# Performance work log

Hardware: AMD Instinct MI355X
Metric: run time of the kernel (lower is better)

The kernel has to match this reference:

```python
import jax, jax.numpy as jnp
import numpy as np

N_NODES = 100000
N_EDGES = 1600000
N_GRAPHS = 1024
TIME_DIM = 64
HID = 32
HEADS = 4
NEG_SLOPE = 0.2


def _gat_layer(x, src, dst, W, a_src, a_dst, bias, heads, out_dim):
    # PyG GATConv: h = x @ W, per-head attention, segment softmax over incoming edges at dst.
    N = x.shape[0]
    h = (x @ W).reshape(N, heads, out_dim)                     # [N, H, D]
    alpha_src = jnp.sum(h * a_src, axis=-1)                    # [N, H]
    alpha_dst = jnp.sum(h * a_dst, axis=-1)                    # [N, H]
    e = alpha_src[src] + alpha_dst[dst]                        # [E, H]
    e = jnp.where(e > 0, e, NEG_SLOPE * e)                     # LeakyReLU(0.2)
    m = jax.ops.segment_max(e, dst, num_segments=N)            # [N, H]
    m = jnp.where(jnp.isfinite(m), m, 0.0)
    ex = jnp.exp(e - m[dst])                                   # [E, H]
    s = jax.ops.segment_sum(ex, dst, num_segments=N)           # [N, H]
    alpha = ex / (s[dst] + 1e-16)                              # [E, H]
    msg = h[src] * alpha[..., None]                            # [E, H, D]
    out = jax.ops.segment_sum(msg, dst, num_segments=N)        # [N, H, D]
    return out.reshape(N, heads * out_dim) + bias


def setup_inputs() -> dict:
    key = jax.random.key(0)
    ks = jax.random.split(key, 12)
    x = jax.random.normal(ks[0], (N_NODES, TIME_DIM), jnp.float32)
    edge_index = jax.random.randint(ks[1], (2, N_EDGES), 0, N_NODES, jnp.int32)
    batch = jnp.sort(jax.random.randint(ks[2], (N_NODES,), 0, N_GRAPHS, jnp.int32))
    s = 0.1
    params = {
        "W1": jax.random.normal(ks[3], (TIME_DIM, HEADS * HID), jnp.float32) * s,
        "a_src1": jax.random.normal(ks[4], (HEADS, HID), jnp.float32) * s,
        "a_dst1": jax.random.normal(ks[5], (HEADS, HID), jnp.float32) * s,
        "b1": jnp.zeros((HEADS * HID,), jnp.float32),
        "W2": jax.random.normal(ks[6], (HEADS * HID, HID), jnp.float32) * s,
        "a_src2": jax.random.normal(ks[7], (1, HID), jnp.float32) * s,
        "a_dst2": jax.random.normal(ks[8], (1, HID), jnp.float32) * s,
        "b2": jnp.zeros((HID,), jnp.float32),
        "Wc": jax.random.normal(ks[9], (HID, 1), jnp.float32) * s,
        "bc": jnp.zeros((1,), jnp.float32),
    }
    return dict(x=x, edge_index=edge_index, batch=batch, **params)


def reference(x, edge_index, batch, W1, a_src1, a_dst1, b1, W2, a_src2, a_dst2, b2, Wc, bc):
    N = x.shape[0]
    # PyG GATConv adds self-loops by default.
    loops = jnp.arange(N, dtype=edge_index.dtype)
    src = jnp.concatenate([edge_index[0], loops])
    dst = jnp.concatenate([edge_index[1], loops])

    h1 = jax.nn.relu(_gat_layer(x, src, dst, W1, a_src1, a_dst1, b1, HEADS, HID))
    h2 = jax.nn.relu(_gat_layer(h1, src, dst, W2, a_src2, a_dst2, b2, 1, HID))

    # global_mean_pool over batch ids
    sums = jax.ops.segment_sum(h2, batch, num_segments=N_GRAPHS)          # [G, HID]
    cnts = jax.ops.segment_sum(jnp.ones((N,), h2.dtype), batch, num_segments=N_GRAPHS)
    pooled = sums / jnp.maximum(cnts, 1.0)[:, None]

    return jax.nn.sigmoid(pooled @ Wc + bc)                               # [G, 1]
```

## Files before the change

### kernel.cpp

```cpp
#include <hip/hip_runtime.h>
#include <hip/hip_bf16.h>

#define BSH 7
#define MAXNB 800
#define STILE 4096
#define BCAP 4096

__device__ inline float bf_lo(unsigned u) { return __uint_as_float(u << 16); }
__device__ inline float bf_hi(unsigned u) { return __uint_as_float(u & 0xffff0000u); }
__device__ inline unsigned bfpack(float x, float y) {
    unsigned lo = (unsigned)__bfloat16_as_ushort(__float2bfloat16(x));
    unsigned hi = ((unsigned)__bfloat16_as_ushort(__float2bfloat16(y))) << 16;
    return lo | hi;
}

__device__ inline void fp4fma(unsigned u, float w, float* a) {
    auto f0 = __builtin_amdgcn_cvt_scalef32_pk_f32_fp4(u, 1.0f, 0);
    auto f1 = __builtin_amdgcn_cvt_scalef32_pk_f32_fp4(u, 1.0f, 1);
    auto f2 = __builtin_amdgcn_cvt_scalef32_pk_f32_fp4(u, 1.0f, 2);
    auto f3 = __builtin_amdgcn_cvt_scalef32_pk_f32_fp4(u, 1.0f, 3);
    a[0] = fmaf(w, f0[0], a[0]); a[1] = fmaf(w, f0[1], a[1]);
    a[2] = fmaf(w, f1[0], a[2]); a[3] = fmaf(w, f1[1], a[3]);
    a[4] = fmaf(w, f2[0], a[4]); a[5] = fmaf(w, f2[1], a[5]);
    a[6] = fmaf(w, f3[0], a[6]); a[7] = fmaf(w, f3[1], a[7]);
}


__global__ __launch_bounds__(256) void k_front(const int* __restrict__ ei, int E, int NB,
                                               int* __restrict__ bcur, int* __restrict__ pairs,
                                               const float* __restrict__ x, const float* __restrict__ W1,
                                               const float* __restrict__ asw, const float* __restrict__ adw,
                                               unsigned* __restrict__ h4, unsigned* __restrict__ aPq,
                                               float2* __restrict__ aDp, int N, int nbsc) {
    __shared__ union USm {
        struct { int lh[MAXNB]; int lbase[MAXNB]; } sc;
        float xt[64][36];
    } sm;
    int t = threadIdx.x;
    if (blockIdx.x < nbsc) {
        int e0 = blockIdx.x * STILE;
        int e1 = min(E, e0 + STILE);
        for (int i = t; i < NB; i += 256) sm.sc.lh[i] = 0;
        __syncthreads();
        int myd[16];
        int q = 0;
        for (int e = e0 + t; e < e1; e += 256, q++) {
            int d = ei[E + e];
            myd[q] = d;
            atomicAdd(&sm.sc.lh[d >> BSH], 1);
        }
        __syncthreads();
        for (int i = t; i < NB; i += 256) {
            int c = sm.sc.lh[i];
            sm.sc.lbase[i] = c ? atomicAdd(&bcur[i], c) : 0;
        }
        __syncthreads();
        for (int i = t; i < NB; i += 256) sm.sc.lh[i] = 0;
        __syncthreads();
        q = 0;
        for (int e = e0 + t; e < e1; e += 256, q++) {
            int s = ei[e];
            int d = myd[q];
            int bk = d >> BSH;
            int off = atomicAdd(&sm.sc.lh[bk], 1);
            pairs[(size_t)bk * BCAP + sm.sc.lbase[bk] + off] = (s << BSH) | (d & ((1 << BSH) - 1));
        }
        return;
    }
    int n0 = (blockIdx.x - nbsc) * 32;
    for (int i = t; i < 32 * 64; i += 256) {
        int r = i >> 6, k = i & 63;
        sm.xt[k][r] = (n0 + r < N) ? x[(size_t)(n0 + r) * 64 + k] : 0.f;
    }
    __syncthreads();
    int cg = t & 31, rg = t >> 5;
    int c0 = cg * 4, r0 = rg * 4;
    int head = c0 >> 5;
    const float* Wp = W1 + c0;
    float acc[4][4];
#pragma unroll
    for (int r = 0; r < 4; r++)
#pragma unroll
        for (int c = 0; c < 4; c++) acc[r][c] = 0.f;
#pragma unroll 4
    for (int k = 0; k < 64; k++) {
        float4 wv = *(const float4*)(Wp + (size_t)k * 128);
        float4 xv = *(const float4*)&sm.xt[k][r0];
        float xr;
        xr = xv.x; acc[0][0]=fmaf(xr,wv.x,acc[0][0]); acc[0][1]=fmaf(xr,wv.y,acc[0][1]); acc[0][2]=fmaf(xr,wv.z,acc[0][2]); acc[0][3]=fmaf(xr,wv.w,acc[0][3]);
        xr = xv.y; acc[1][0]=fmaf(xr,wv.x,acc[1][0]); acc[1][1]=fmaf(xr,wv.y,acc[1][1]); acc[1][2]=fmaf(xr,wv.z,acc[1][2]); acc[1][3]=fmaf(xr,wv.w,acc[1][3]);
        xr = xv.z; acc[2][0]=fmaf(xr,wv.x,acc[2][0]); acc[2][1]=fmaf(xr,wv.y,acc[2][1]); acc[2][2]=fmaf(xr,wv.z,acc[2][2]); acc[2][3]=fmaf(xr,wv.w,acc[2][3]);
        xr = xv.w; acc[3][0]=fmaf(xr,wv.x,acc[3][0]); acc[3][1]=fmaf(xr,wv.y,acc[3][1]); acc[3][2]=fmaf(xr,wv.z,acc[3][2]); acc[3][3]=fmaf(xr,wv.w,acc[3][3]);
    }
#pragma unroll
    for (int r = 0; r < 4; r++) {
        int n = n0 + r0 + r;
        if (n < N) {
            unsigned u = __builtin_amdgcn_cvt_scalef32_pk_fp4_f32(0u, acc[r][0], acc[r][1], 1.0f, 0);
            u = __builtin_amdgcn_cvt_scalef32_pk_fp4_f32(u, acc[r][2], acc[r][3], 1.0f, 1);
            ((unsigned short*)h4)[(size_t)n * 32 + cg] = (unsigned short)(u & 0xffffu);
        }
    }
    float4 awv = *(const float4*)(asw + c0);
    float4 dwv = *(const float4*)(adw + c0);
#pragma unroll
    for (int r = 0; r < 4; r++) {
        float as = acc[r][0] * awv.x + acc[r][1] * awv.y + acc[r][2] * awv.z + acc[r][3] * awv.w;
        float ad = acc[r][0] * dwv.x + acc[r][1] * dwv.y + acc[r][2] * dwv.z + acc[r][3] * dwv.w;
#pragma unroll
        for (int m = 1; m < 8; m <<= 1) { as += __shfl_xor(as, m); ad += __shfl_xor(ad, m); }
        int n = n0 + r0 + r;
        if ((t & 7) == 0 && n < N) {
            aPq[n * 4 + head] = bfpack(__expf(as), __expf(0.2f * as));
            aDp[n * 4 + head] = make_float2(__expf(ad), __expf(0.2f * ad));
        }
    }
}


__global__ __launch_bounds__(256) void k_build(const int* __restrict__ pairs,
                                               const int* __restrict__ bcur, int N, int NB,
                                               int2* __restrict__ span, int* __restrict__ csr) {
    __shared__ int lcnt[128];
    __shared__ int loff[128];
    __shared__ int lcur[128];
    int b = blockIdx.x, t = threadIdx.x;
    int node0 = b << BSH;
    size_t base = (size_t)b * BCAP;
    int ne = bcur[b];
    if (t < 128) lcnt[t] = 0;
    __syncthreads();
    for (int i = t; i < ne; i += 256) atomicAdd(&lcnt[pairs[base + i] & 127], 1);
    __syncthreads();
    if (t < 128) loff[t] = lcnt[t];
    __syncthreads();
#pragma unroll
    for (int off = 1; off < 128; off <<= 1) {
        int v = (t < 128 && t >= off) ? loff[t - off] : 0;
        __syncthreads();
        if (t < 128) loff[t] += v;
        __syncthreads();
    }
    if (t < 128) {
        int excl = loff[t] - lcnt[t];
        int n = node0 + t;
        if (n < N) span[n] = make_int2((int)base + excl, (int)base + excl + lcnt[t]);
        lcur[t] = excl;
    }
    __syncthreads();
    for (int i = t; i < ne; i += 256) {
        int p = pairs[base + i];
        int pos = (int)base + atomicAdd(&lcur[p & 127], 1);
        csr[pos] = ((unsigned)p) >> BSH;
    }
}


__global__ __launch_bounds__(256) void k_gat1(const unsigned* __restrict__ h4,
                                              const unsigned* __restrict__ aPq, const float2* __restrict__ aDp,
                                              const int2* __restrict__ span, const int* __restrict__ csr,
                                              const float* __restrict__ b1, unsigned* __restrict__ out, int N) {
    int t = threadIdx.x;
    int n = blockIdx.x * 4 + (t >> 6);
    if (n >= N) return;
    int lane = t & 63;
    int e4 = lane >> 4, c = lane & 15;
    int head = c >> 2;
    float2 dnp = aDp[n * 4 + head];
    float ec = dnp.x, ed = dnp.y;
    unsigned apn = aPq[n * 4 + head];
    float w_self = fmaxf(bf_lo(apn) * ec, bf_hi(apn) * ed);
    int2 sp = span[n];
    int beg = sp.x, end = sp.y;

    float a[8] = {0, 0, 0, 0, 0, 0, 0, 0};
    float s = 0.f;
    if (e4 == 0) {
        fp4fma(h4[(size_t)n * 16 + c], w_self, a);
        s = w_self;
    }
    int j = beg + e4;
    for (; j + 4 < end; j += 8) {
        int s0 = csr[j], s1 = csr[j + 4];
        unsigned ap0 = aPq[s0 * 4 + head], ap1 = aPq[s1 * 4 + head];
        unsigned u0 = h4[(size_t)s0 * 16 + c];
        unsigned u1 = h4[(size_t)s1 * 16 + c];
        float w0 = fmaxf(bf_lo(ap0) * ec, bf_hi(ap0) * ed);
        float w1 = fmaxf(bf_lo(ap1) * ec, bf_hi(ap1) * ed);
        s += w0 + w1;
        fp4fma(u0, w0, a);
        fp4fma(u1, w1, a);
    }
    for (; j < end; j += 4) {
        int sj = csr[j];
        unsigned ap = aPq[sj * 4 + head];
        unsigned u = h4[(size_t)sj * 16 + c];
        float w = fmaxf(bf_lo(ap) * ec, bf_hi(ap) * ed);
        s += w;
        fp4fma(u, w, a);
    }
#pragma unroll
    for (int off = 16; off < 64; off <<= 1) {
#pragma unroll
        for (int i = 0; i < 8; i++) a[i] += __shfl_xor(a[i], off);
        s += __shfl_xor(s, off);
    }
    if (e4 == 0) {
        float inv = 1.f / (s + 1e-16f);
        float4 ba = ((const float4*)b1)[c * 2];
        float4 bb = ((const float4*)b1)[c * 2 + 1];
        float o0 = fmaxf(fmaf(a[0], inv, ba.x), 0.f);
        float o1 = fmaxf(fmaf(a[1], inv, ba.y), 0.f);
        float o2 = fmaxf(fmaf(a[2], inv, ba.z), 0.f);
        float o3 = fmaxf(fmaf(a[3], inv, ba.w), 0.f);
        float o4 = fmaxf(fmaf(a[4], inv, bb.x), 0.f);
        float o5 = fmaxf(fmaf(a[5], inv, bb.y), 0.f);
        float o6 = fmaxf(fmaf(a[6], inv, bb.z), 0.f);
        float o7 = fmaxf(fmaf(a[7], inv, bb.w), 0.f);
        uint4 o;
        o.x = bfpack(o0, o1); o.y = bfpack(o2, o3);
        o.z = bfpack(o4, o5); o.w = bfpack(o6, o7);
        ((uint4*)out)[(size_t)n * 16 + c] = o;
    }
}


__global__ __launch_bounds__(256) void k_gemm2(const unsigned* __restrict__ h1b, const float* __restrict__ W2,
                                               const float* __restrict__ asw, const float* __restrict__ adw,
                                               unsigned short* __restrict__ h4b, unsigned* __restrict__ aPq,
                                               float2* __restrict__ aDp, int N) {
    __shared__ float xt[128][36];
    int t = threadIdx.x;
    int n0 = blockIdx.x * 32;
    for (int i = t; i < 32 * 64; i += 256) {
        int r = i >> 6, c = i & 63;
        unsigned u = (n0 + r < N) ? h1b[(size_t)(n0 + r) * 64 + c] : 0u;
        xt[2 * c][r]     = bf_lo(u);
        xt[2 * c + 1][r] = bf_hi(u);
    }
    __syncthreads();
    int cg = t & 7, rg = t >> 3;
    int c0 = cg * 4;
    const float* Wp = W2 + c0;
    float a0 = 0.f, a1 = 0.f, a2 = 0.f, a3 = 0.f;
#pragma unroll 4
    for (int k = 0; k < 128; k++) {
        float4 wv = *(const float4*)(Wp + (size_t)k * 32);
        float xr = xt[k][rg];
        a0 = fmaf(xr, wv.x, a0); a1 = fmaf(xr, wv.y, a1);
        a2 = fmaf(xr, wv.z, a2); a3 = fmaf(xr, wv.w, a3);
    }
    int n = n0 + rg;
    if (n < N) {
        unsigned u = __builtin_amdgcn_cvt_scalef32_pk_fp4_f32(0u, a0, a1, 1.0f, 0);
        u = __builtin_amdgcn_cvt_scalef32_pk_fp4_f32(u, a2, a3, 1.0f, 1);
        h4b[(size_t)n * 8 + cg] = (unsigned short)(u & 0xffffu);
    }
    float4 awv = *(const float4*)(asw + c0);
    float4 dwv = *(const float4*)(adw + c0);
    float as = a0 * awv.x + a1 * awv.y + a2 * awv.z + a3 * awv.w;
    float ad = a0 * dwv.x + a1 * dwv.y + a2 * dwv.z + a3 * dwv.w;
#pragma unroll
    for (int m = 1; m < 8; m <<= 1) { as += __shfl_xor(as, m); ad += __shfl_xor(ad, m); }
    if (cg == 0 && n < N) {
        aPq[n] = bfpack(__expf(as), __expf(0.2f * as));
        aDp[n] = make_float2(__expf(ad), __expf(0.2f * ad));
    }
}


__global__ __launch_bounds__(256) void k_gat2(const unsigned* __restrict__ h4,
                                              const unsigned* __restrict__ aPq, const float2* __restrict__ aDp,
                                              const int2* __restrict__ span, const int* __restrict__ csr,
                                              const float* __restrict__ b2, float* __restrict__ out, int N) {
    int t = threadIdx.x;
    int n = blockIdx.x * 4 + (t >> 6);
    if (n >= N) return;
    int lane = t & 63;
    int e16 = lane >> 2, c = lane & 3;
    float2 dnp = aDp[n];
    float ec = dnp.x, ed = dnp.y;
    unsigned apn = aPq[n];
    float w_self = fmaxf(bf_lo(apn) * ec, bf_hi(apn) * ed);
    int2 sp = span[n];
    int beg = sp.x, end = sp.y;

    float a[8] = {0, 0, 0, 0, 0, 0, 0, 0};
    float s = 0.f;
    if (e16 == 0) {
        fp4fma(h4[(size_t)n * 4 + c], w_self, a);
        s = w_self;
    }
    int j = beg + e16;
    for (; j + 16 < end; j += 32) {
        int s0 = csr[j], s1 = csr[j + 16];
        unsigned ap0 = aPq[s0], ap1 = aPq[s1];
        unsigned u0 = h4[(size_t)s0 * 4 + c];
        unsigned u1 = h4[(size_t)s1 * 4 + c];
        float w0 = fmaxf(bf_lo(ap0) * ec, bf_hi(ap0) * ed);
        float w1 = fmaxf(bf_lo(ap1) * ec, bf_hi(ap1) * ed);
        s += w0 + w1;
        fp4fma(u0, w0, a);
        fp4fma(u1, w1, a);
    }
    for (; j < end; j += 16) {
        int sj = csr[j];
        unsigned ap = aPq[sj];
        unsigned u = h4[(size_t)sj * 4 + c];
        float w = fmaxf(bf_lo(ap) * ec, bf_hi(ap) * ed);
        s += w;
        fp4fma(u, w, a);
    }
#pragma unroll
    for (int off = 4; off < 64; off <<= 1) {
#pragma unroll
        for (int i = 0; i < 8; i++) a[i] += __shfl_xor(a[i], off);
        s += __shfl_xor(s, off);
    }
    if (e16 == 0) {
        float inv = 1.f / (s + 1e-16f);
        float4 ba = ((const float4*)b2)[c * 2];
        float4 bb = ((const float4*)b2)[c * 2 + 1];
        float4 oa, ob;
        oa.x = fmaxf(fmaf(a[0], inv, ba.x), 0.f);
        oa.y = fmaxf(fmaf(a[1], inv, ba.y), 0.f);
        oa.z = fmaxf(fmaf(a[2], inv, ba.z), 0.f);
        oa.w = fmaxf(fmaf(a[3], inv, ba.w), 0.f);
        ob.x = fmaxf(fmaf(a[4], inv, bb.x), 0.f);
        ob.y = fmaxf(fmaf(a[5], inv, bb.y), 0.f);
        ob.z = fmaxf(fmaf(a[6], inv, bb.z), 0.f);
        ob.w = fmaxf(fmaf(a[7], inv, bb.w), 0.f);
        ((float4*)out)[(size_t)n * 8 + c * 2]     = oa;
        ((float4*)out)[(size_t)n * 8 + c * 2 + 1] = ob;
    }
}


__global__ void k_pool(const float* __restrict__ h2r, const int* __restrict__ batch, int N,
                       const float* __restrict__ Wc, const float* __restrict__ bc,
                       float* __restrict__ out) {
    int g = blockIdx.x;
    int t = threadIdx.x, d = t & 31, r = t >> 5;
    int lo = 0, hi = N;
    while (lo < hi) { int mid = (lo + hi) >> 1; if (batch[mid] < g) lo = mid + 1; else hi = mid; }
    int start = lo;
    hi = N;
    while (lo < hi) { int mid = (lo + hi) >> 1; if (batch[mid] < g + 1) lo = mid + 1; else hi = mid; }
    int end = lo;
    float sum = 0.f;
    for (int i = start + r; i < end; i += 2) sum += h2r[(size_t)i * 32 + d];
    sum += __shfl_xor(sum, 32);
    float cnt = (float)(end - start);
    float mean = sum / fmaxf(cnt, 1.f);
    float v = mean * Wc[d];
#pragma unroll
    for (int m = 16; m >= 1; m >>= 1) v += __shfl_xor(v, m);
    if (t == 0) out[g] = 1.f / (1.f + expf(-(v + bc[0])));
}


extern "C" void kernel_launch(void* const* d_in, const int* in_sizes, int n_in,
                              void* d_out, int out_size, void* d_ws, size_t ws_size,
                              hipStream_t stream) {
    const float* x    = (const float*)d_in[0];
    const int*   ei   = (const int*)d_in[1];
    const int*   batch= (const int*)d_in[2];
    const float* W1   = (const float*)d_in[3];
    const float* as1  = (const float*)d_in[4];
    const float* ad1  = (const float*)d_in[5];
    const float* b1   = (const float*)d_in[6];
    const float* W2   = (const float*)d_in[7];
    const float* as2  = (const float*)d_in[8];
    const float* ad2  = (const float*)d_in[9];
    const float* b2   = (const float*)d_in[10];
    const float* Wc   = (const float*)d_in[11];
    const float* bc   = (const float*)d_in[12];

    const int N = in_sizes[0] / 64;
    const int E = in_sizes[1] / 2;
    const int G = out_size;
    const int NB = (N + 127) >> BSH;

    size_t off = 0;
    char* base = (char*)d_ws;
    auto alloc = [&](size_t bytes) -> char* {
        char* p = base + off;
        off += (bytes + 255) & ~(size_t)255;
        return p;
    };
    int*      bcur  = (int*)alloc((size_t)NB * 4);
    int*      pairs = (int*)alloc((size_t)NB * BCAP * 4);
    int2*     span  = (int2*)alloc((size_t)N * 8);
    int*      csr   = (int*)alloc((size_t)NB * BCAP * 4);
    unsigned* h4_1  = (unsigned*)alloc((size_t)N * 64);
    unsigned* h1b   = (unsigned*)alloc((size_t)N * 64 * 4);
    unsigned* aPq1  = (unsigned*)alloc((size_t)N * 4 * 4);
    float2*   aDp1  = (float2*)alloc((size_t)N * 4 * 8);
    unsigned short* h4_2 = (unsigned short*)alloc((size_t)N * 16);
    unsigned* aPq2  = (unsigned*)alloc((size_t)N * 4);
    float2*   aDp2  = (float2*)alloc((size_t)N * 8);
    float*    h2r   = (float*)alloc((size_t)N * 32 * 4);
    (void)ws_size; (void)n_in;

    const int nbsc = (E + STILE - 1) / STILE;

    hipMemsetAsync(bcur, 0, (size_t)NB * 4, stream);

    k_front<<<nbsc + (N + 31) / 32, 256, 0, stream>>>(ei, E, NB, bcur, pairs,
                                                      x, W1, as1, ad1, h4_1, aPq1, aDp1, N, nbsc);
    k_build<<<NB, 256, 0, stream>>>(pairs, bcur, N, NB, span, csr);

    k_gat1<<<(N + 3) / 4, 256, 0, stream>>>(h4_1, aPq1, aDp1, span, csr, b1, h1b, N);

    k_gemm2<<<(N + 31) / 32, 256, 0, stream>>>(h1b, W2, as2, ad2, h4_2, aPq2, aDp2, N);
    k_gat2<<<(N + 3) / 4, 256, 0, stream>>>((const unsigned*)h4_2, aPq2, aDp2, span, csr, b2, h2r, N);

    k_pool<<<G, 64, 0, stream>>>(h2r, batch, N, Wc, bc, (float*)d_out);
}
```

Baseline: 247.9 us.

## Split fused scatter/GEMM front kernel and double edge tile size

Splits the combined bucket-scatter and layer-1 GEMM kernel into two separate kernels, launching the GEMM after the CSR build instead of alongside the scatter. It also doubles the per-block edge tile from 4096 to 8192, which halves the number of scatter blocks and the global atomics on bucket counters. The trade-off is the lost overlap between scatter and GEMM blocks plus one extra launch. The larger myd register array (32 entries) may raise register pressure and lower occupancy in the scatter kernel.

```diff
diff --git a/kernel.cpp b/kernel.cpp
--- a/kernel.cpp
+++ b/kernel.cpp
@@ -3,7 +3,7 @@
 
 #define BSH 7
 #define MAXNB 800
-#define STILE 4096
+#define STILE 8192
 #define BCAP 4096
 
 __device__ inline float bf_lo(unsigned u) { return __uint_as_float(u << 16); }
@@ -26,51 +26,51 @@
 }
 
 
-__global__ __launch_bounds__(256) void k_front(const int* __restrict__ ei, int E, int NB,
-                                               int* __restrict__ bcur, int* __restrict__ pairs,
-                                               const float* __restrict__ x, const float* __restrict__ W1,
+__global__ __launch_bounds__(256) void k_bscatter(const int* __restrict__ ei, int E, int NB,
+                                                  int* __restrict__ bcur, int* __restrict__ pairs) {
+    __shared__ int lh[MAXNB];
+    __shared__ int lbase[MAXNB];
+    int t = threadIdx.x;
+    int e0 = blockIdx.x * STILE;
+    int e1 = min(E, e0 + STILE);
+    for (int i = t; i < NB; i += 256) lh[i] = 0;
+    __syncthreads();
+    int myd[32];
+    int q = 0;
+    for (int e = e0 + t; e < e1; e += 256, q++) {
+        int d = ei[E + e];
+        myd[q] = d;
+        atomicAdd(&lh[d >> BSH], 1);
+    }
+    __syncthreads();
+    for (int i = t; i < NB; i += 256) {
+        int c = lh[i];
+        lbase[i] = c ? atomicAdd(&bcur[i], c) : 0;
+    }
+    __syncthreads();
+    for (int i = t; i < NB; i += 256) lh[i] = 0;
+    __syncthreads();
+    q = 0;
+    for (int e = e0 + t; e < e1; e += 256, q++) {
+        int s = ei[e];
+        int d = myd[q];
+        int bk = d >> BSH;
+        int off = atomicAdd(&lh[bk], 1);
+        pairs[(size_t)bk * BCAP + lbase[bk] + off] = (s << BSH) | (d & ((1 << BSH) - 1));
+    }
+}
+
+
+__global__ __launch_bounds__(256) void k_gemm1(const float* __restrict__ x, const float* __restrict__ W1,
                                                const float* __restrict__ asw, const float* __restrict__ adw,
                                                unsigned* __restrict__ h4, unsigned* __restrict__ aPq,
-                                               float2* __restrict__ aDp, int N, int nbsc) {
-    __shared__ union USm {
-        struct { int lh[MAXNB]; int lbase[MAXNB]; } sc;
-        float xt[64][36];
-    } sm;
+                                               float2* __restrict__ aDp, int N) {
+    __shared__ float xt[64][36];
     int t = threadIdx.x;
-    if (blockIdx.x < nbsc) {
-        int e0 = blockIdx.x * STILE;
-        int e1 = min(E, e0 + STILE);
-        for (int i = t; i < NB; i += 256) sm.sc.lh[i] = 0;
-        __syncthreads();
-        int myd[16];
-        int q = 0;
-        for (int e = e0 + t; e < e1; e += 256, q++) {
-            int d = ei[E + e];
-            myd[q] = d;
-            atomicAdd(&sm.sc.lh[d >> BSH], 1);
-        }
-        __syncthreads();
-        for (int i = t; i < NB; i += 256) {
-            int c = sm.sc.lh[i];
-            sm.sc.lbase[i] = c ? atomicAdd(&bcur[i], c) : 0;
-        }
-        __syncthreads();
-        for (int i = t; i < NB; i += 256) sm.sc.lh[i] = 0;
-        __syncthreads();
-        q = 0;
-        for (int e = e0 + t; e < e1; e += 256, q++) {
-            int s = ei[e];
-            int d = myd[q];
-            int bk = d >> BSH;
-            int off = atomicAdd(&sm.sc.lh[bk], 1);
-            pairs[(size_t)bk * BCAP + sm.sc.lbase[bk] + off] = (s << BSH) | (d & ((1 << BSH) - 1));
-        }
-        return;
-    }
-    int n0 = (blockIdx.x - nbsc) * 32;
+    int n0 = blockIdx.x * 32;
     for (int i = t; i < 32 * 64; i += 256) {
         int r = i >> 6, k = i & 63;
-        sm.xt[k][r] = (n0 + r < N) ? x[(size_t)(n0 + r) * 64 + k] : 0.f;
+        xt[k][r] = (n0 + r < N) ? x[(size_t)(n0 + r) * 64 + k] : 0.f;
     }
     __syncthreads();
     int cg = t & 31, rg = t >> 5;
@@ -85,7 +85,7 @@
 #pragma unroll 4
     for (int k = 0; k < 64; k++) {
         float4 wv = *(const float4*)(Wp + (size_t)k * 128);
-        float4 xv = *(const float4*)&sm.xt[k][r0];
+        float4 xv = *(const float4*)&xt[k][r0];
         float xr;
         xr = xv.x; acc[0][0]=fmaf(xr,wv.x,acc[0][0]); acc[0][1]=fmaf(xr,wv.y,acc[0][1]); acc[0][2]=fmaf(xr,wv.z,acc[0][2]); acc[0][3]=fmaf(xr,wv.w,acc[0][3]);
         xr = xv.y; acc[1][0]=fmaf(xr,wv.x,acc[1][0]); acc[1][1]=fmaf(xr,wv.y,acc[1][1]); acc[1][2]=fmaf(xr,wv.z,acc[1][2]); acc[1][3]=fmaf(xr,wv.w,acc[1][3]);
@@ -402,14 +402,12 @@
     float*    h2r   = (float*)alloc((size_t)N * 32 * 4);
     (void)ws_size; (void)n_in;
 
-    const int nbsc = (E + STILE - 1) / STILE;
-
     hipMemsetAsync(bcur, 0, (size_t)NB * 4, stream);
 
-    k_front<<<nbsc + (N + 31) / 32, 256, 0, stream>>>(ei, E, NB, bcur, pairs,
-                                                      x, W1, as1, ad1, h4_1, aPq1, aDp1, N, nbsc);
+    k_bscatter<<<(E + STILE - 1) / STILE, 256, 0, stream>>>(ei, E, NB, bcur, pairs);
     k_build<<<NB, 256, 0, stream>>>(pairs, bcur, N, NB, span, csr);
 
+    k_gemm1<<<(N + 31) / 32, 256, 0, stream>>>(x, W1, as1, ad1, h4_1, aPq1, aDp1, N);
     k_gat1<<<(N + 3) / 4, 256, 0, stream>>>(h4_1, aPq1, aDp1, span, csr, b1, h1b, N);
 
     k_gemm2<<<(N + 31) / 32, 256, 0, stream>>>(h1b, W2, as2, ad2, h4_2, aPq2, aDp2, N);
```

Result: slower. 259.7 us (+4.8%).
